# Optimization experiments

Measured on AMD Instinct MI355X. Metric: run time of the kernel, lower is better.

The kernel has to match this reference:

```python
import jax, jax.numpy as jnp
import numpy as np

N = 100000      # nodes
E = 1600000     # edges (before self-loops)
F_IN = 256      # input features
H = 8           # heads, layer 1
FH = 8          # features per head, layer 1
C = 64          # n_classes (layer 2 out, heads=1)
SLOPE = 0.2     # leaky relu negative slope


def setup_inputs() -> dict:
    key = jax.random.key(0)
    ks = jax.random.split(key, 12)
    x = jax.random.normal(ks[0], (N, F_IN), jnp.float32)
    edge_index = jax.random.randint(ks[1], (2, E), 0, N, dtype=jnp.int32)
    # scalar edge weights in [0.5, 1.5) so the (1 - 1/w) correction is well-behaved
    edge_weight = jax.random.uniform(ks[2], (E,), jnp.float32, 0.5, 1.5)
    W1 = jax.random.normal(ks[3], (F_IN, H * FH), jnp.float32) / np.sqrt(F_IN)
    att_src1 = jax.random.normal(ks[4], (H, FH), jnp.float32) * 0.1
    att_dst1 = jax.random.normal(ks[5], (H, FH), jnp.float32) * 0.1
    b1 = jnp.zeros((H * FH,), jnp.float32)
    W2 = jax.random.normal(ks[6], (H * FH, C), jnp.float32) / np.sqrt(H * FH)
    att_src2 = jax.random.normal(ks[7], (1, C), jnp.float32) * 0.1
    att_dst2 = jax.random.normal(ks[8], (1, C), jnp.float32) * 0.1
    b2 = jnp.zeros((C,), jnp.float32)
    return {"x": x, "edge_index": edge_index, "edge_weight": edge_weight,
            "W1": W1, "att_src1": att_src1, "att_dst1": att_dst1, "b1": b1,
            "W2": W2, "att_src2": att_src2, "att_dst2": att_dst2, "b2": b2}


def _gat_layer(x, src, dst, ew, W, a_src, a_dst, b, heads, fph, concat):
    n = x.shape[0]
    h = (x @ W).reshape(n, heads, fph)                      # [N,H,F]
    al_src = jnp.sum(h * a_src, axis=-1)                    # [N,H]
    al_dst = jnp.sum(h * a_dst, axis=-1)                    # [N,H]
    alpha = jax.nn.leaky_relu(al_src[src] + al_dst[dst], SLOPE)  # [E,H]
    alpha = alpha + (1.0 - 1.0 / ew)[:, None]               # scalar edge-weight correction
    # segment softmax over destination nodes
    m = jax.ops.segment_max(alpha, dst, num_segments=n)
    e = jnp.exp(alpha - m[dst])
    s = jax.ops.segment_sum(e, dst, num_segments=n)
    alpha = e / (s[dst] + 1e-16)                            # [E,H]
    msg = h[src] * alpha[:, :, None]                        # [E,H,F]
    out = jax.ops.segment_sum(msg, dst, num_segments=n)     # [N,H,F]
    out = out.reshape(n, heads * fph) if concat else out.mean(axis=1)
    return out + b


def reference(x, edge_index, edge_weight, W1, att_src1, att_dst1, b1,
              W2, att_src2, att_dst2, b2):
    n = x.shape[0]
    loops = jnp.arange(n, dtype=edge_index.dtype)
    src = jnp.concatenate([edge_index[0], loops])
    dst = jnp.concatenate([edge_index[1], loops])
    ew = jnp.concatenate([edge_weight, jnp.ones((n,), edge_weight.dtype)])  # fill_value=1.0
    # dropout layers are identity in eval mode
    h = _gat_layer(x, src, dst, ew, W1, att_src1, att_dst1, b1, H, FH, concat=True)
    h = jax.nn.elu(h)
    out = _gat_layer(h, src, dst, ew, W2, att_src2, att_dst2, b2, 1, C, concat=False)
    return out
```

## Files before the change

### kernel.cpp

```cpp
#include <hip/hip_runtime.h>
#include <math.h>

#define NNODES 100000
#define NEDGES 1600000
#define EATOT  1700000
#define FIN    256
#define C1     64
#define NH     8
#define C2     64
#define SLOPE  0.2f
#define LOG2E  1.4426950408889634f
#define QSCALE 8192.0f

#define NBKT  391
#define BCAP  5120
#define EPB_A 4096
#define NBLK_A 416

#define NT1 3125
#define NT2 1563
#define GGRID 512

typedef __attribute__((ext_vector_type(8))) short short8;
typedef __attribute__((ext_vector_type(4))) float f32x4;

__device__ __forceinline__ void edge_sdc(int e, const int* __restrict__ ei,
                                         const float* __restrict__ ew,
                                         int& s, int& d, float& corr){
  if (e < NEDGES){ s = ei[e]; d = ei[NEDGES + e]; corr = 1.0f - 1.0f / ew[e]; }
  else { s = e - NEDGES; d = s; corr = 0.0f; }
}

__device__ __forceinline__ unsigned short f2bf(float f){
  unsigned u = __float_as_uint(f);
  unsigned r = (u + 0x7FFFu + ((u >> 16) & 1u)) >> 16;
  return (unsigned short)r;
}

__global__ void k_zero_gc(int* __restrict__ gcount){
  int t = threadIdx.x;
  if (t < NBKT) gcount[t] = 0;
}

__global__ __launch_bounds__(256) void k_bucketA(
    const int* __restrict__ ei, const float* __restrict__ ew,
    int* __restrict__ gcount, uint2* __restrict__ brec){
  __shared__ int cnt[NBKT];
  __shared__ int base[NBKT];
  int t = threadIdx.x;
  for (int i = t; i < NBKT; i += 256) cnt[i] = 0;
  __syncthreads();
  int e0 = blockIdx.x * EPB_A;
  int e1 = e0 + EPB_A; if (e1 > EATOT) e1 = EATOT;
  for (int e = e0 + t; e < e1; e += 256){
    int d = (e < NEDGES) ? ei[NEDGES + e] : (e - NEDGES);
    atomicAdd(&cnt[d >> 8], 1);
  }
  __syncthreads();
  for (int i = t; i < NBKT; i += 256){
    int c = cnt[i];
    base[i] = c ? atomicAdd(&gcount[i], c) : 0;
    cnt[i] = 0;
  }
  __syncthreads();
  for (int e = e0 + t; e < e1; e += 256){
    int s, d; float corr;
    edge_sdc(e, ei, ew, s, d, corr);
    int bkt = d >> 8;
    int rel = base[bkt] + atomicAdd(&cnt[bkt], 1);
    int q = __float2int_rn(corr * (LOG2E * QSCALE));
    unsigned packed = ((unsigned)q << 17) | (unsigned)s;
    brec[(size_t)bkt * BCAP + rel] = make_uint2((unsigned)d, packed);
  }
}

__global__ void k_bucketS(const int* __restrict__ gcount, int* __restrict__ gbase,
                          int* __restrict__ rowptr){
  __shared__ int sh[512];
  int t = threadIdx.x;
  int v = (t < NBKT) ? gcount[t] : 0;
  sh[t] = v; __syncthreads();
  for (int off = 1; off < 512; off <<= 1){
    int y = (t >= off) ? sh[t - off] : 0;
    __syncthreads();
    sh[t] += y;
    __syncthreads();
  }
  if (t < NBKT) gbase[t] = sh[t] - v;
  if (t == 0) rowptr[NNODES] = EATOT;
}

__global__ __launch_bounds__(256) void k_bucketB(
    const uint2* __restrict__ brec, const int* __restrict__ gcount,
    const int* __restrict__ gbase, int* __restrict__ rowptr, int* __restrict__ rec){
  __shared__ int hist[256];
  __shared__ int scanb[256];
  __shared__ int excl[256];
  __shared__ int cur[256];
  int bkt = blockIdx.x;
  int t = threadIdx.x;
  int n0 = bkt << 8;
  int cnt = gcount[bkt];
  int gb = gbase[bkt];
  hist[t] = 0;
  __syncthreads();
  const uint2* breg = brec + (size_t)bkt * BCAP;
  for (int j = t; j < cnt; j += 256)
    atomicAdd(&hist[breg[j].x & 255u], 1);
  __syncthreads();
  int h = hist[t];
  scanb[t] = h;
  __syncthreads();
  for (int off = 1; off < 256; off <<= 1){
    int y = (t >= off) ? scanb[t - off] : 0;
    __syncthreads();
    scanb[t] += y;
    __syncthreads();
  }
  int ex = scanb[t] - h;
  excl[t] = ex;
  cur[t] = 0;
  if (n0 + t < NNODES) rowptr[n0 + t] = gb + ex;
  __syncthreads();
  for (int j = t; j < cnt; j += 256){
    uint2 r = breg[j];
    int dl = (int)(r.x & 255u);
    int pos = gb + excl[dl] + atomicAdd(&cur[dl], 1);
    rec[pos] = (int)r.y;
  }
}

__global__ void k_splitw(const float* __restrict__ W, short* __restrict__ th,
                         short* __restrict__ tl, int K){
  int idx = blockIdx.x * blockDim.x + threadIdx.x;
  if (idx >= K * 64) return;
  int k = idx >> 6, c = idx & 63;
  float w = W[idx];
  unsigned int b = __float_as_uint(w);
  unsigned short h = (unsigned short)(b >> 16);
  float hf = __uint_as_float(b & 0xffff0000u);
  float rem = w - hf;
  unsigned short lo = (unsigned short)(__float_as_uint(rem) >> 16);
  th[c * K + k] = (short)h;
  tl[c * K + k] = (short)lo;
}

__global__ __launch_bounds__(256, 2) void k_gemm1(
    const float* __restrict__ X, const short* __restrict__ Bth,
    const short* __restrict__ Btl, const float* __restrict__ asrc,
    const float* __restrict__ adst, unsigned short* __restrict__ Hout,
    float* __restrict__ alsrc, float* __restrict__ aldst)
{
  __shared__ float xbuf[2][32 * 256];
  const int lane = threadIdx.x & 63;
  const int wave = threadIdx.x >> 6;
  const int l15 = lane & 15;
  const int kg = lane >> 4;
  const int cp = wave & 1;
  const int rh = wave >> 1;
  const int rl = rh * 16 + l15;
  const int rs = rl & 7;

  short8 bh[8][2], bl[8][2];
  #pragma unroll
  for (int ks = 0; ks < 8; ++ks){
    #pragma unroll
    for (int cc = 0; cc < 2; ++cc){
      unsigned boff = (unsigned)((cp * 2 + cc) * 16 + l15) * FIN + ks * 32 + kg * 8;
      bh[ks][cc] = *(const short8*)&Bth[boff];
      bl[ks][cc] = *(const short8*)&Btl[boff];
    }
  }
  float ascv[2], adcv[2];
  #pragma unroll
  for (int cc = 0; cc < 2; ++cc){
    ascv[cc] = asrc[(cp * 2 + cc) * 16 + l15] * LOG2E;
    adcv[cc] = adst[(cp * 2 + cc) * 16 + l15] * LOG2E;
  }

  const int t0 = blockIdx.x;
  #pragma unroll
  for (int t = 0; t < 8; ++t){
    int r = wave * 8 + t;
    unsigned u = (unsigned)(lane ^ (r & 7));
    __builtin_amdgcn_global_load_lds(
        (const unsigned int*)(X + (size_t)(t0 * 32 + r) * FIN + u * 4),
        (unsigned int*)&xbuf[0][r * 256], 16, 0, 0);
  }

  int cur = 0;
  for (int ti = t0; ti < NT1; ti += GGRID){
    __syncthreads();
    int nxt = ti + GGRID;
    if (nxt < NT1){
      #pragma unroll
      for (int t = 0; t < 8; ++t){
        int r = wave * 8 + t;
        unsigned u = (unsigned)(lane ^ (r & 7));
        __builtin_amdgcn_global_load_lds(
            (const unsigned int*)(X + (size_t)(nxt * 32 + r) * FIN + u * 4),
            (unsigned int*)&xbuf[cur ^ 1][r * 256], 16, 0, 0);
      }
    }

    f32x4 acc[2] = {f32x4{0,0,0,0}, f32x4{0,0,0,0}};
    #pragma unroll
    for (int ks = 0; ks < 8; ++ks){
      int k0 = ks * 32 + kg * 8;
      unsigned U = (unsigned)(k0 >> 2);
      float4 xa = *(const float4*)&xbuf[cur][rl * 256 + ((U ^ rs) << 2)];
      float4 xb = *(const float4*)&xbuf[cur][rl * 256 + (((U + 1) ^ rs) << 2)];
      float xs[8] = {xa.x, xa.y, xa.z, xa.w, xb.x, xb.y, xb.z, xb.w};
      short8 ah, al;
      #pragma unroll
      for (int j = 0; j < 8; ++j){
        unsigned u = __float_as_uint(xs[j]);
        ah[j] = (short)(u >> 16);
        float hf = __uint_as_float(u & 0xffff0000u);
        al[j] = (short)(__float_as_uint(xs[j] - hf) >> 16);
      }
      #pragma unroll
      for (int cc = 0; cc < 2; ++cc){
        acc[cc] = __builtin_amdgcn_mfma_f32_16x16x32_bf16(ah, bh[ks][cc], acc[cc], 0, 0, 0);
        acc[cc] = __builtin_amdgcn_mfma_f32_16x16x32_bf16(ah, bl[ks][cc], acc[cc], 0, 0, 0);
        acc[cc] = __builtin_amdgcn_mfma_f32_16x16x32_bf16(al, bh[ks][cc], acc[cc], 0, 0, 0);
      }
    }

    int rowg = ti * 32 + rh * 16 + kg * 4;
    #pragma unroll
    for (int cc = 0; cc < 2; ++cc){
      #pragma unroll
      for (int reg = 0; reg < 4; ++reg)
        Hout[(size_t)(rowg + reg) * 64 + (cp * 2 + cc) * 16 + l15] = f2bf(acc[cc][reg]);
    }
    #pragma unroll
    for (int reg = 0; reg < 4; ++reg){
      int r = rowg + reg;
      #pragma unroll
      for (int cc = 0; cc < 2; ++cc){
        float ps = acc[cc][reg] * ascv[cc];
        float pd = acc[cc][reg] * adcv[cc];
        ps += __shfl_xor(ps, 1, 64); ps += __shfl_xor(ps, 2, 64); ps += __shfl_xor(ps, 4, 64);
        pd += __shfl_xor(pd, 1, 64); pd += __shfl_xor(pd, 2, 64); pd += __shfl_xor(pd, 4, 64);
        if ((l15 & 7) == 0){
          int head = (cp * 2 + cc) * 2 + (l15 >> 3);
          alsrc[r * NH + head] = ps;
          aldst[r * NH + head] = pd;
        }
      }
    }
    cur ^= 1;
  }
}

__global__ __launch_bounds__(256, 2) void k_gemm2(
    const unsigned short* __restrict__ Ah, const unsigned short* __restrict__ Al,
    const short* __restrict__ Bth, const short* __restrict__ Btl,
    const float* __restrict__ asrc, const float* __restrict__ adst,
    unsigned short* __restrict__ Hout, float* __restrict__ alsrc,
    float* __restrict__ aldst)
{
  __shared__ unsigned short abuf[2][2][64 * 64];
  const int lane = threadIdx.x & 63;
  const int wave = threadIdx.x >> 6;
  const int l15 = lane & 15;
  const int kg = lane >> 4;
  const int rl = wave * 16 + l15;
  const int rs = rl & 7;

  short8 bh[2][4], bl[2][4];
  #pragma unroll
  for (int ks = 0; ks < 2; ++ks){
    #pragma unroll
    for (int c = 0; c < 4; ++c){
      unsigned boff = (unsigned)(c * 16 + l15) * C1 + ks * 32 + kg * 8;
      bh[ks][c] = *(const short8*)&Bth[boff];
      bl[ks][c] = *(const short8*)&Btl[boff];
    }
  }
  float ascv[4], adcv[4];
  #pragma unroll
  for (int c = 0; c < 4; ++c){
    ascv[c] = asrc[c * 16 + l15] * LOG2E;
    adcv[c] = adst[c * 16 + l15] * LOG2E;
  }

  const int t0 = blockIdx.x;
  auto stage = [&](int buf, int tile){
    #pragma unroll
    for (int j = 0; j < 4; ++j){
      int q = wave * 4 + j;
      int p = q >> 3, rb = q & 7;
      int r = rb * 8 + (lane >> 3);
      int rg = tile * 64 + r; if (rg > NNODES - 1) rg = NNODES - 1;
      unsigned u = (unsigned)((lane & 7) ^ (lane >> 3));
      const unsigned short* src = (p ? Al : Ah) + (size_t)rg * 64 + u * 8;
      __builtin_amdgcn_global_load_lds(
          (const unsigned int*)src,
          (unsigned int*)&abuf[buf][p][rb * 512], 16, 0, 0);
    }
  };
  stage(0, t0);

  int cur = 0;
  for (int ti = t0; ti < NT2; ti += GGRID){
    __syncthreads();
    int nxt = ti + GGRID;
    if (nxt < NT2) stage(cur ^ 1, nxt);

    f32x4 acc[4] = {f32x4{0,0,0,0}, f32x4{0,0,0,0}, f32x4{0,0,0,0}, f32x4{0,0,0,0}};
    #pragma unroll
    for (int ks = 0; ks < 2; ++ks){
      unsigned U = (unsigned)(ks * 4 + kg);
      short8 ah = *(const short8*)&abuf[cur][0][rl * 64 + ((U ^ rs) << 3)];
      short8 al = *(const short8*)&abuf[cur][1][rl * 64 + ((U ^ rs) << 3)];
      #pragma unroll
      for (int c = 0; c < 4; ++c){
        acc[c] = __builtin_amdgcn_mfma_f32_16x16x32_bf16(ah, bh[ks][c], acc[c], 0, 0, 0);
        acc[c] = __builtin_amdgcn_mfma_f32_16x16x32_bf16(ah, bl[ks][c], acc[c], 0, 0, 0);
        acc[c] = __builtin_amdgcn_mfma_f32_16x16x32_bf16(al, bh[ks][c], acc[c], 0, 0, 0);
      }
    }

    int rowg = ti * 64 + wave * 16 + kg * 4;
    #pragma unroll
    for (int c = 0; c < 4; ++c){
      #pragma unroll
      for (int reg = 0; reg < 4; ++reg){
        int r = rowg + reg;
        if (r < NNODES) Hout[(size_t)r * 64 + c * 16 + l15] = f2bf(acc[c][reg]);
      }
    }
    #pragma unroll
    for (int reg = 0; reg < 4; ++reg){
      int r = rowg + reg;
      float ps = 0.0f, pd = 0.0f;
      #pragma unroll
      for (int c = 0; c < 4; ++c){
        ps = fmaf(acc[c][reg], ascv[c], ps);
        pd = fmaf(acc[c][reg], adcv[c], pd);
      }
      ps += __shfl_xor(ps, 1, 64); ps += __shfl_xor(ps, 2, 64);
      ps += __shfl_xor(ps, 4, 64); ps += __shfl_xor(ps, 8, 64);
      pd += __shfl_xor(pd, 1, 64); pd += __shfl_xor(pd, 2, 64);
      pd += __shfl_xor(pd, 4, 64); pd += __shfl_xor(pd, 8, 64);
      if (l15 == 0 && r < NNODES){ alsrc[r] = ps; aldst[r] = pd; }
    }
    cur ^= 1;
  }
}

template<int HEADS, bool DO_ELU, bool SPLIT_OUT>
__global__ __launch_bounds__(256) void k_agg(
    const int* __restrict__ rec, const int* __restrict__ rowptr,
    const unsigned short* __restrict__ hbuf,
    const float* __restrict__ alsrc, const float* __restrict__ aldst,
    const float* __restrict__ bias, float* __restrict__ outF,
    unsigned short* __restrict__ outH, unsigned short* __restrict__ outL){
  int tid = blockIdx.x * blockDim.x + threadIdx.x;
  int d = tid >> 6;
  int c = threadIdx.x & 63;
  if (d >= NNODES) return;
  d = __builtin_amdgcn_readfirstlane(d);
  int beg = rowptr[d], end = rowptr[d + 1];
  int h = (HEADS == 8) ? (c >> 3) : 0;
  float ad = aldst[(size_t)d * HEADS + h];
  float s = 0.0f, acc = 0.0f;

  auto body = [&](int w, float a, float hv){
    float v = a + ad;
    v = fmaxf(v, v * SLOPE);
    v += (float)(w >> 17) * (1.0f / QSCALE);
    v = fminf(v, 60.0f);
    float e = __builtin_amdgcn_exp2f(v);
    s += e;
    acc = fmaf(e, hv, acc);
  };

  int j = beg;
  for (; j + 8 <= end; j += 8){
    int w[8]; float a[8], hv[8];
    #pragma unroll
    for (int i = 0; i < 8; ++i) w[i] = rec[j + i];
    #pragma unroll
    for (int i = 0; i < 8; ++i){
      unsigned si = (unsigned)w[i] & 0x1FFFFu;
      a[i] = alsrc[si * HEADS + h];
      hv[i] = __uint_as_float((unsigned)hbuf[si * 64 + c] << 16);
    }
    #pragma unroll
    for (int i = 0; i < 8; ++i) body(w[i], a[i], hv[i]);
  }
  for (; j < end; ++j){
    int w = rec[j];
    unsigned sj = (unsigned)w & 0x1FFFFu;
    float a = alsrc[sj * HEADS + h];
    float hv = __uint_as_float((unsigned)hbuf[sj * 64 + c] << 16);
    body(w, a, hv);
  }

  float o = acc / (s + 1e-16f) + bias[c];
  if (DO_ELU) o = (o > 0.0f) ? o : (__expf(o) - 1.0f);
  if (SPLIT_OUT){
    unsigned u = __float_as_uint(o);
    outH[(size_t)d * 64 + c] = (unsigned short)(u >> 16);
    float hf = __uint_as_float(u & 0xffff0000u);
    outL[(size_t)d * 64 + c] = (unsigned short)(__float_as_uint(o - hf) >> 16);
  } else {
    outF[(size_t)d * 64 + c] = o;
  }
}

extern "C" void kernel_launch(void* const* d_in, const int* in_sizes, int n_in,
                              void* d_out, int out_size, void* d_ws, size_t ws_size,
                              hipStream_t stream) {
  const float* x    = (const float*)d_in[0];
  const int*   ei   = (const int*)d_in[1];
  const float* ew   = (const float*)d_in[2];
  const float* W1   = (const float*)d_in[3];
  const float* as1  = (const float*)d_in[4];
  const float* ad1  = (const float*)d_in[5];
  const float* b1   = (const float*)d_in[6];
  const float* W2   = (const float*)d_in[7];
  const float* as2  = (const float*)d_in[8];
  const float* ad2  = (const float*)d_in[9];
  const float* b2   = (const float*)d_in[10];
  float* dout = (float*)d_out;

  float* ws = (float*)d_ws;
  size_t off = 0;
  auto alloc = [&](size_t nfloats) -> float* {
    float* p = ws + off;
    off += (nfloats + 15) & ~(size_t)15;
    return p;
  };
  unsigned short* h1 = (unsigned short*)alloc((size_t)NNODES * C1 / 2);
  unsigned short* o1h = (unsigned short*)alloc((size_t)NNODES * C1 / 2);
  unsigned short* o1l = (unsigned short*)alloc((size_t)NNODES * C1 / 2);
  float* alsrc1  = alloc((size_t)NNODES * NH);
  float* aldst1  = alloc((size_t)NNODES * NH);
  float* alsrc2  = alloc(NNODES);
  float* aldst2  = alloc(NNODES);
  int*   gcount  = (int*)alloc(NBKT + 16);
  int*   gbase   = (int*)alloc(NBKT + 16);
  int*   rowptr  = (int*)alloc(NNODES + 1);
  int*   rec     = (int*)alloc(EATOT);
  uint2* brec    = (uint2*)alloc((size_t)NBKT * BCAP * 2);
  short* wt1h    = (short*)alloc(64 * FIN / 2);
  short* wt1l    = (short*)alloc(64 * FIN / 2);
  short* wt2h    = (short*)alloc(64 * C1 / 2);
  short* wt2l    = (short*)alloc(64 * C1 / 2);
  unsigned short* h2 = h1;

  const int BS = 256;

  hipLaunchKernelGGL(k_splitw, dim3((FIN * 64 + BS - 1) / BS), dim3(BS), 0, stream,
                     W1, wt1h, wt1l, FIN);
  hipLaunchKernelGGL(k_splitw, dim3((C1 * 64 + BS - 1) / BS), dim3(BS), 0, stream,
                     W2, wt2h, wt2l, C1);

  hipLaunchKernelGGL(k_zero_gc, dim3(1), dim3(512), 0, stream, gcount);
  hipLaunchKernelGGL(k_bucketA, dim3(NBLK_A), dim3(BS), 0, stream, ei, ew, gcount, brec);
  hipLaunchKernelGGL(k_bucketS, dim3(1), dim3(512), 0, stream, gcount, gbase, rowptr);
  hipLaunchKernelGGL(k_bucketB, dim3(NBKT), dim3(BS), 0, stream,
                     brec, gcount, gbase, rowptr, rec);

  int agrid = (NNODES * 64 + BS - 1) / BS;

  hipLaunchKernelGGL(k_gemm1, dim3(GGRID), dim3(BS), 0, stream,
                     x, wt1h, wt1l, as1, ad1, h1, alsrc1, aldst1);
  hipLaunchKernelGGL((k_agg<NH, true, true>), dim3(agrid), dim3(BS), 0, stream,
                     rec, rowptr, h1, alsrc1, aldst1, b1, (float*)nullptr, o1h, o1l);

  hipLaunchKernelGGL(k_gemm2, dim3(GGRID), dim3(BS), 0, stream,
                     o1h, o1l, wt2h, wt2l, as2, ad2, h2, alsrc2, aldst2);
  hipLaunchKernelGGL((k_agg<1, false, false>), dim3(agrid), dim3(BS), 0, stream,
                     rec, rowptr, h2, alsrc2, aldst2, b2, dout,
                     (unsigned short*)nullptr, (unsigned short*)nullptr);
}
```

Measured before the change: 221.5 us.

## Merge setup kernels, register-cache bucketA edges, co-launch bucketB with gemm1

Folds the two weight-split kernels and the bucket-counter zeroing into a single pre kernel, which cuts the launch count. bucketA now reads each edge once into registers (16 per thread) and reuses them in the scatter pass instead of reloading from global memory. The per-bucket CSR build (bucketB) is merged into the gemm1 launch as extra leading blocks, so the independent sort and GEMM work can run concurrently on the GPU. Possible costs are higher register pressure in bucketA and the launch-bounds occupancy hint of 2 now applying to the bucket blocks.

```diff
diff --git a/kernel.cpp b/kernel.cpp
--- a/kernel.cpp
+++ b/kernel.cpp
@@ -24,22 +24,38 @@
 typedef __attribute__((ext_vector_type(8))) short short8;
 typedef __attribute__((ext_vector_type(4))) float f32x4;
 
-__device__ __forceinline__ void edge_sdc(int e, const int* __restrict__ ei,
-                                         const float* __restrict__ ew,
-                                         int& s, int& d, float& corr){
-  if (e < NEDGES){ s = ei[e]; d = ei[NEDGES + e]; corr = 1.0f - 1.0f / ew[e]; }
-  else { s = e - NEDGES; d = s; corr = 0.0f; }
-}
-
 __device__ __forceinline__ unsigned short f2bf(float f){
   unsigned u = __float_as_uint(f);
   unsigned r = (u + 0x7FFFu + ((u >> 16) & 1u)) >> 16;
   return (unsigned short)r;
 }
 
-__global__ void k_zero_gc(int* __restrict__ gcount){
-  int t = threadIdx.x;
-  if (t < NBKT) gcount[t] = 0;
+__device__ __forceinline__ void splitw_body(const float* __restrict__ W,
+                                            short* __restrict__ th, short* __restrict__ tl,
+                                            int K, int idx){
+  int k = idx >> 6, c = idx & 63;
+  float w = W[idx];
+  unsigned int b = __float_as_uint(w);
+  unsigned short h = (unsigned short)(b >> 16);
+  float hf = __uint_as_float(b & 0xffff0000u);
+  float rem = w - hf;
+  unsigned short lo = (unsigned short)(__float_as_uint(rem) >> 16);
+  th[c * K + k] = (short)h;
+  tl[c * K + k] = (short)lo;
+}
+
+__global__ void k_pre(const float* __restrict__ W1, short* __restrict__ w1h,
+                      short* __restrict__ w1l, const float* __restrict__ W2,
+                      short* __restrict__ w2h, short* __restrict__ w2l,
+                      int* __restrict__ gcount){
+  int b = blockIdx.x, t = threadIdx.x;
+  if (b < 64){
+    splitw_body(W1, w1h, w1l, FIN, b * 256 + t);
+  } else if (b < 80){
+    splitw_body(W2, w2h, w2l, C1, (b - 64) * 256 + t);
+  } else {
+    for (int i = t; i < NBKT; i += 256) gcount[i] = 0;
+  }
 }
 
 __global__ __launch_bounds__(256) void k_bucketA(
@@ -52,9 +68,21 @@
   __syncthreads();
   int e0 = blockIdx.x * EPB_A;
   int e1 = e0 + EPB_A; if (e1 > EATOT) e1 = EATOT;
-  for (int e = e0 + t; e < e1; e += 256){
-    int d = (e < NEDGES) ? ei[NEDGES + e] : (e - NEDGES);
-    atomicAdd(&cnt[d >> 8], 1);
+
+  int dv[16]; unsigned pv[16];
+  #pragma unroll
+  for (int i = 0; i < 16; ++i){
+    int e = e0 + t + i * 256;
+    dv[i] = -1;
+    if (e < e1){
+      int s, d; float corr;
+      if (e < NEDGES){ s = ei[e]; d = ei[NEDGES + e]; corr = 1.0f - 1.0f / ew[e]; }
+      else { s = e - NEDGES; d = s; corr = 0.0f; }
+      int q = __float2int_rn(corr * (LOG2E * QSCALE));
+      dv[i] = d;
+      pv[i] = ((unsigned)q << 17) | (unsigned)s;
+      atomicAdd(&cnt[d >> 8], 1);
+    }
   }
   __syncthreads();
   for (int i = t; i < NBKT; i += 256){
@@ -63,14 +91,13 @@
     cnt[i] = 0;
   }
   __syncthreads();
-  for (int e = e0 + t; e < e1; e += 256){
-    int s, d; float corr;
-    edge_sdc(e, ei, ew, s, d, corr);
-    int bkt = d >> 8;
-    int rel = base[bkt] + atomicAdd(&cnt[bkt], 1);
-    int q = __float2int_rn(corr * (LOG2E * QSCALE));
-    unsigned packed = ((unsigned)q << 17) | (unsigned)s;
-    brec[(size_t)bkt * BCAP + rel] = make_uint2((unsigned)d, packed);
+  #pragma unroll
+  for (int i = 0; i < 16; ++i){
+    if (dv[i] >= 0){
+      int bkt = dv[i] >> 8;
+      int rel = base[bkt] + atomicAdd(&cnt[bkt], 1);
+      brec[(size_t)bkt * BCAP + rel] = make_uint2((unsigned)dv[i], pv[i]);
+    }
   }
 }
 
@@ -90,68 +117,55 @@
   if (t == 0) rowptr[NNODES] = EATOT;
 }
 
-__global__ __launch_bounds__(256) void k_bucketB(
+__global__ __launch_bounds__(256, 2) void k_bg1(
     const uint2* __restrict__ brec, const int* __restrict__ gcount,
-    const int* __restrict__ gbase, int* __restrict__ rowptr, int* __restrict__ rec){
-  __shared__ int hist[256];
-  __shared__ int scanb[256];
-  __shared__ int excl[256];
-  __shared__ int cur[256];
-  int bkt = blockIdx.x;
-  int t = threadIdx.x;
-  int n0 = bkt << 8;
-  int cnt = gcount[bkt];
-  int gb = gbase[bkt];
-  hist[t] = 0;
-  __syncthreads();
-  const uint2* breg = brec + (size_t)bkt * BCAP;
-  for (int j = t; j < cnt; j += 256)
-    atomicAdd(&hist[breg[j].x & 255u], 1);
-  __syncthreads();
-  int h = hist[t];
-  scanb[t] = h;
-  __syncthreads();
-  for (int off = 1; off < 256; off <<= 1){
-    int y = (t >= off) ? scanb[t - off] : 0;
-    __syncthreads();
-    scanb[t] += y;
-    __syncthreads();
-  }
-  int ex = scanb[t] - h;
-  excl[t] = ex;
-  cur[t] = 0;
-  if (n0 + t < NNODES) rowptr[n0 + t] = gb + ex;
-  __syncthreads();
-  for (int j = t; j < cnt; j += 256){
-    uint2 r = breg[j];
-    int dl = (int)(r.x & 255u);
-    int pos = gb + excl[dl] + atomicAdd(&cur[dl], 1);
-    rec[pos] = (int)r.y;
-  }
-}
-
-__global__ void k_splitw(const float* __restrict__ W, short* __restrict__ th,
-                         short* __restrict__ tl, int K){
-  int idx = blockIdx.x * blockDim.x + threadIdx.x;
-  if (idx >= K * 64) return;
-  int k = idx >> 6, c = idx & 63;
-  float w = W[idx];
-  unsigned int b = __float_as_uint(w);
-  unsigned short h = (unsigned short)(b >> 16);
-  float hf = __uint_as_float(b & 0xffff0000u);
-  float rem = w - hf;
-  unsigned short lo = (unsigned short)(__float_as_uint(rem) >> 16);
-  th[c * K + k] = (short)h;
-  tl[c * K + k] = (short)lo;
-}
-
-__global__ __launch_bounds__(256, 2) void k_gemm1(
+    const int* __restrict__ gbase, int* __restrict__ rowptr, int* __restrict__ rec,
     const float* __restrict__ X, const short* __restrict__ Bth,
     const short* __restrict__ Btl, const float* __restrict__ asrc,
     const float* __restrict__ adst, unsigned short* __restrict__ Hout,
     float* __restrict__ alsrc, float* __restrict__ aldst)
 {
   __shared__ float xbuf[2][32 * 256];
+
+  if (blockIdx.x < NBKT){
+    int* hist  = (int*)&xbuf[0][0];
+    int* scanb = hist + 256;
+    int* excl  = scanb + 256;
+    int* cur   = excl + 256;
+    int bkt = blockIdx.x;
+    int t = threadIdx.x;
+    int n0 = bkt << 8;
+    int cnt = gcount[bkt];
+    int gb = gbase[bkt];
+    hist[t] = 0;
+    __syncthreads();
+    const uint2* breg = brec + (size_t)bkt * BCAP;
+    for (int j = t; j < cnt; j += 256)
+      atomicAdd(&hist[breg[j].x & 255u], 1);
+    __syncthreads();
+    int h = hist[t];
+    scanb[t] = h;
+    __syncthreads();
+    for (int off = 1; off < 256; off <<= 1){
+      int y = (t >= off) ? scanb[t - off] : 0;
+      __syncthreads();
+      scanb[t] += y;
+      __syncthreads();
+    }
+    int ex = scanb[t] - h;
+    excl[t] = ex;
+    cur[t] = 0;
+    if (n0 + t < NNODES) rowptr[n0 + t] = gb + ex;
+    __syncthreads();
+    for (int j = t; j < cnt; j += 256){
+      uint2 r = breg[j];
+      int dl = (int)(r.x & 255u);
+      int pos = gb + excl[dl] + atomicAdd(&cur[dl], 1);
+      rec[pos] = (int)r.y;
+    }
+    return;
+  }
+
   const int lane = threadIdx.x & 63;
   const int wave = threadIdx.x >> 6;
   const int l15 = lane & 15;
@@ -178,7 +192,7 @@
     adcv[cc] = adst[(cp * 2 + cc) * 16 + l15] * LOG2E;
   }
 
-  const int t0 = blockIdx.x;
+  const int t0 = blockIdx.x - NBKT;
   #pragma unroll
   for (int t = 0; t < 8; ++t){
     int r = wave * 8 + t;
@@ -455,21 +469,18 @@
 
   const int BS = 256;
 
-  hipLaunchKernelGGL(k_splitw, dim3((FIN * 64 + BS - 1) / BS), dim3(BS), 0, stream,
-                     W1, wt1h, wt1l, FIN);
-  hipLaunchKernelGGL(k_splitw, dim3((C1 * 64 + BS - 1) / BS), dim3(BS), 0, stream,
-                     W2, wt2h, wt2l, C1);
-
-  hipLaunchKernelGGL(k_zero_gc, dim3(1), dim3(512), 0, stream, gcount);
+  hipLaunchKernelGGL(k_pre, dim3(81), dim3(BS), 0, stream,
+                     W1, wt1h, wt1l, W2, wt2h, wt2l, gcount);
+
   hipLaunchKernelGGL(k_bucketA, dim3(NBLK_A), dim3(BS), 0, stream, ei, ew, gcount, brec);
   hipLaunchKernelGGL(k_bucketS, dim3(1), dim3(512), 0, stream, gcount, gbase, rowptr);
-  hipLaunchKernelGGL(k_bucketB, dim3(NBKT), dim3(BS), 0, stream,
-                     brec, gcount, gbase, rowptr, rec);
+
+  hipLaunchKernelGGL(k_bg1, dim3(NBKT + GGRID), dim3(BS), 0, stream,
+                     brec, gcount, gbase, rowptr, rec,
+                     x, wt1h, wt1l, as1, ad1, h1, alsrc1, aldst1);
 
   int agrid = (NNODES * 64 + BS - 1) / BS;
 
-  hipLaunchKernelGGL(k_gemm1, dim3(GGRID), dim3(BS), 0, stream,
-                     x, wt1h, wt1l, as1, ad1, h1, alsrc1, aldst1);
   hipLaunchKernelGGL((k_agg<NH, true, true>), dim3(agrid), dim3(BS), 0, stream,
                      rec, rowptr, h1, alsrc1, aldst1, b1, (float*)nullptr, o1h, o1l);
 
```

New measurement: 212.9 us. 3.9% less time.
